# Performance work log

Measured on AMD Instinct MI355X. Metric: run time of the kernel, lower is better.

Reference implementation:

```python
import jax, jax.numpy as jnp
import numpy as np

FEAT_STRIDE = 16
NEG_OV, POS_OV = 0.3, 0.7
RPN_BATCH = 256
NUM_FG = int(0.5 * RPN_BATCH)  # RPN_FG_FRACTION * RPN_BATCHSIZE


def _gen_anchors(base=16, ratios=(0.5, 1.0, 2.0), scales=(4, 8, 16)):
    # 3D extension of the classic generate_anchors: ratio warps w/h, scale multiplies all dims
    ctr = (base - 1) / 2.0
    rows = []
    for r in ratios:
        for s in scales:
            w = base * s * np.sqrt(1.0 / r)
            h = base * s * np.sqrt(r)
            d = float(base * s)
            rows.append([ctr - 0.5 * (w - 1), ctr - 0.5 * (h - 1),
                         ctr + 0.5 * (w - 1), ctr + 0.5 * (h - 1),
                         ctr - 0.5 * (d - 1), ctr + 0.5 * (d - 1)])
    return np.asarray(rows, np.float32)


def setup_inputs() -> dict:
    key = jax.random.key(0)
    ks = jax.random.split(key, 8)
    B, H, W, D, K, A = 2, 48, 48, 24, 20, 9
    cls = jax.random.normal(ks[0], (B, 2 * A, H, W, D), jnp.float32)
    x1 = jax.random.uniform(ks[1], (B, K)) * 600.0
    y1 = jax.random.uniform(ks[2], (B, K)) * 600.0
    z1 = jax.random.uniform(ks[3], (B, K)) * 300.0
    whd = 16.0 + jax.random.uniform(ks[4], (B, K, 3)) * jnp.array([104.0, 104.0, 48.0])
    x2 = jnp.minimum(x1 + whd[..., 0], 767.0)
    y2 = jnp.minimum(y1 + whd[..., 1], 767.0)
    z2 = jnp.minimum(z1 + whd[..., 2], 383.0)
    cid = jax.random.randint(ks[5], (B, K), 1, 4).astype(jnp.float32)
    gt_boxes = jnp.stack([x1, y1, x2, y2, z1, z2, cid], axis=2)
    im_info = jnp.tile(jnp.array([[768.0, 768.0, 384.0]], jnp.float32), (B, 1))
    total = H * W * D * A
    return {
        'rpn_cls_score': cls,
        'gt_boxes': gt_boxes,
        'im_info': im_info,
        'num_boxes': jnp.full((B,), K, jnp.int32),
        'anchors': jnp.asarray(_gen_anchors()),
        'rand_fg': jax.random.uniform(ks[6], (B, total)),
        'rand_bg': jax.random.uniform(ks[7], (B, total)),
    }


def _overlaps(anc, gt):
    # anc: (N,6) [x1,y1,x2,y2,z1,z2]; gt: (B,K,7) -> IoU (B,N,K)
    aw = anc[:, 2] - anc[:, 0] + 1.0
    ah = anc[:, 3] - anc[:, 1] + 1.0
    ad = anc[:, 5] - anc[:, 4] + 1.0
    a_area = aw * ah * ad  # (N,)
    gw = gt[:, :, 2] - gt[:, :, 0] + 1.0
    gh = gt[:, :, 3] - gt[:, :, 1] + 1.0
    gd = gt[:, :, 5] - gt[:, :, 4] + 1.0
    g_area = gw * gh * gd  # (B,K)
    iw = jnp.clip(jnp.minimum(anc[None, :, None, 2], gt[:, None, :, 2]) -
                  jnp.maximum(anc[None, :, None, 0], gt[:, None, :, 0]) + 1.0, 0.0)
    ih = jnp.clip(jnp.minimum(anc[None, :, None, 3], gt[:, None, :, 3]) -
                  jnp.maximum(anc[None, :, None, 1], gt[:, None, :, 1]) + 1.0, 0.0)
    idp = jnp.clip(jnp.minimum(anc[None, :, None, 5], gt[:, None, :, 5]) -
                   jnp.maximum(anc[None, :, None, 4], gt[:, None, :, 4]) + 1.0, 0.0)
    inter = iw * ih * idp
    ov = inter / (a_area[None, :, None] + g_area[:, None, :] - inter)
    gt_zero = (gw == 1.0) & (gh == 1.0) & (gd == 1.0)
    a_zero = (aw == 1.0) & (ah == 1.0) & (ad == 1.0)
    ov = jnp.where(gt_zero[:, None, :], 0.0, ov)
    ov = jnp.where(a_zero[None, :, None], -1.0, ov)
    return ov


def _transform(ex, gt):
    # ex: (N,6); gt: (B,N,6) -> (B,N,6) targets (dx,dy,dz,dw,dh,dd)
    ew = ex[:, 2] - ex[:, 0] + 1.0
    eh = ex[:, 3] - ex[:, 1] + 1.0
    ed = ex[:, 5] - ex[:, 4] + 1.0
    ecx = ex[:, 0] + 0.5 * (ew - 1.0)
    ecy = ex[:, 1] + 0.5 * (eh - 1.0)
    ecz = ex[:, 4] + 0.5 * (ed - 1.0)
    gw = gt[:, :, 2] - gt[:, :, 0] + 1.0
    gh = gt[:, :, 3] - gt[:, :, 1] + 1.0
    gd = gt[:, :, 5] - gt[:, :, 4] + 1.0
    gcx = gt[:, :, 0] + 0.5 * (gw - 1.0)
    gcy = gt[:, :, 1] + 0.5 * (gh - 1.0)
    gcz = gt[:, :, 4] + 0.5 * (gd - 1.0)
    return jnp.stack([(gcx - ecx[None]) / ew[None],
                      (gcy - ecy[None]) / eh[None],
                      (gcz - ecz[None]) / ed[None],
                      jnp.log(gw / ew[None]),
                      jnp.log(gh / eh[None]),
                      jnp.log(gd / ed[None])], axis=2)


def _rank(p):
    # rank of each element when sorted by descending priority, per row
    return jnp.argsort(jnp.argsort(-p, axis=1), axis=1)


def reference(rpn_cls_score, gt_boxes, im_info, num_boxes, anchors, rand_fg, rand_bg):
    B = gt_boxes.shape[0]
    H, W, D = rpn_cls_score.shape[2], rpn_cls_score.shape[3], rpn_cls_score.shape[4]
    A = anchors.shape[0]
    sx = jnp.arange(W, dtype=jnp.float32) * FEAT_STRIDE
    sy = jnp.arange(H, dtype=jnp.float32) * FEAT_STRIDE
    sz = jnp.arange(D, dtype=jnp.float32) * FEAT_STRIDE
    mx, my, mz = jnp.meshgrid(sx, sy, sz, indexing='xy')  # (H,W,D) each
    shifts = jnp.stack([mx.ravel(), my.ravel(), mx.ravel(), my.ravel(), mz.ravel(), mz.ravel()], axis=1)
    all_anchors = (anchors[None, :, :] + shifts[:, None, :]).reshape(-1, 6)  # (total,6)
    total = all_anchors.shape[0]
    inside = ((all_anchors[:, 0] >= 0) & (all_anchors[:, 1] >= 0) & (all_anchors[:, 4] >= 0) &
              (all_anchors[:, 2] < im_info[0, 1]) & (all_anchors[:, 3] < im_info[0, 0]) &
              (all_anchors[:, 5] < im_info[0, 2]))  # (total,)

    ov = _overlaps(all_anchors, gt_boxes)                       # (B,total,K)
    ov_m = jnp.where(inside[None, :, None], ov, -1.0)           # mask outside anchors
    max_ov = ov_m.max(axis=2)
    argmax_ov = jnp.argmax(ov_m, axis=2)                        # (B,total)

    labels = jnp.full((B, total), -1.0, jnp.float32)
    ins = inside[None, :]
    labels = jnp.where(ins & (max_ov < NEG_OV), 0.0, labels)
    gt_max = ov_m.max(axis=1)                                   # (B,K)
    gt_max = jnp.where(gt_max == 0.0, 1e-5, gt_max)
    tie = jnp.sum(ov_m == gt_max[:, None, :], axis=2) > 0
    labels = jnp.where(ins & tie, 1.0, labels)
    labels = jnp.where(ins & (max_ov >= POS_OV), 1.0, labels)

    # fg subsampling: randomly keep at most NUM_FG positives per image
    fg = labels == 1.0
    rk = _rank(jnp.where(fg, rand_fg, -1.0))
    labels = jnp.where(fg & (rk >= NUM_FG), -1.0, labels)
    # bg subsampling: keep RPN_BATCH - num_fg negatives per image
    num_bg = RPN_BATCH - jnp.sum(labels == 1.0, axis=1)         # (B,)
    bg = labels == 0.0
    rkb = _rank(jnp.where(bg, rand_bg, -1.0))
    labels = jnp.where(bg & (rkb >= num_bg[:, None]), -1.0, labels)

    assigned = jnp.take_along_axis(gt_boxes, argmax_ov[:, :, None], axis=1)  # (B,total,7)
    bbox_targets = _transform(all_anchors, assigned[:, :, :6])
    bbox_targets = jnp.where(inside[None, :, None], bbox_targets, 0.0)

    in_w = jnp.where(labels == 1.0, 1.0, 0.0)                   # RPN_BBOX_INSIDE_WEIGHTS[0]=1
    # replicate original bug: weights from the LAST image's example count
    num_examples = jnp.sum(labels[-1] >= 0.0).astype(jnp.float32)
    w = 1.0 / num_examples
    out_w = jnp.where(labels == 1.0, w, jnp.where(labels == 0.0, w, 0.0))

    labels_o = labels.reshape(B, H, W, D, A).transpose(0, 4, 1, 2, 3).reshape(B, 1, A * H * D, W)
    bt_o = bbox_targets.reshape(B, H, W, D, A * 6).transpose(0, 4, 1, 2, 3)
    iw_o = jnp.broadcast_to(in_w[:, :, None], (B, total, 6)).reshape(B, H, W, D, 6 * A).transpose(0, 4, 1, 2, 3)
    ow_o = jnp.broadcast_to(out_w[:, :, None], (B, total, 6)).reshape(B, H, W, D, 6 * A).transpose(0, 4, 1, 2, 3)
    return labels_o, bt_o, iw_o, ow_o
```

## Files before the change

### kernel.cpp

```cpp
#include <hip/hip_runtime.h>
#include <math.h>

#define BB 2
#define HH 48
#define WW 48
#define DD 24
#define KK 20
#define AA 9
#define TOTAL (HH*WW*DD*AA)
#define SPAT (HH*WW*DD)
#define OUT0N (BB*TOTAL)
#define CH 54
#define NB 4096
#define CAP 4096
#define FG_QUOTA 128
#define RPN_B 256
#define STRIDE_F 16.0f

#define O_ARGMAX 0
#define O_GTMAX  (OUT0N)
#define O_HIST   (O_GTMAX + BB*KK)
#define O_CUT    (O_HIST + 4*NB)
#define O_TIEN   (O_CUT + 12)
#define O_TIE    (O_TIEN + 4)
#define O_W      (O_TIE + 4*CAP)

__device__ __forceinline__ unsigned enc_f(float f){
  unsigned u = __float_as_uint(f);
  return (u & 0x80000000u) ? ~u : (u | 0x80000000u);
}
__device__ __forceinline__ float dec_f(unsigned u){
  return (u & 0x80000000u) ? __uint_as_float(u & 0x7FFFFFFFu) : __uint_as_float(~u);
}
#define ENC_NEG1 0x407FFFFFu

__device__ __forceinline__ float iou6(float ax1,float ay1,float ax2,float ay2,
                                      float az1,float az2, const float* g){
  #pragma clang fp contract(off)
  float aw = ax2-ax1+1.0f, ah = ay2-ay1+1.0f, ad = az2-az1+1.0f;
  float a_area = aw*ah*ad;
  float gw = g[2]-g[0]+1.0f, gh = g[3]-g[1]+1.0f, gd = g[5]-g[4]+1.0f;
  float g_area = gw*gh*gd;
  float iw = fminf(ax2,g[2]) - fmaxf(ax1,g[0]) + 1.0f; iw = fmaxf(iw,0.0f);
  float ih = fminf(ay2,g[3]) - fmaxf(ay1,g[1]) + 1.0f; ih = fmaxf(ih,0.0f);
  float id = fminf(az2,g[5]) - fmaxf(az1,g[4]) + 1.0f; id = fmaxf(id,0.0f);
  float inter = iw*ih*id;
  float ov = inter / (a_area + g_area - inter);
  if (gw==1.0f && gh==1.0f && gd==1.0f) ov = 0.0f;
  if (aw==1.0f && ah==1.0f && ad==1.0f) ov = -1.0f;
  return ov;
}

__global__ void k_init(unsigned* __restrict__ ws){
  int t = blockIdx.x*256 + threadIdx.x;
  if (t < 4*NB) ws[O_HIST + t] = 0u;
  if (t < 4)    ws[O_TIEN + t] = 0u;
  if (t < BB*KK) ws[O_GTMAX + t] = ENC_NEG1;
}

#define GM_G 8
#define GM_BLK 243
__global__ void __launch_bounds__(256) k_gtmax(const float* __restrict__ gt,
    const float* __restrict__ anc, const float* __restrict__ imi,
    unsigned* __restrict__ ws){
  __shared__ float s_gt[KK*7];
  __shared__ float s_anc[AA*6];
  __shared__ float s_im[3];
  __shared__ unsigned s_max[KK];
  int tid = threadIdx.x;
  int b = blockIdx.y;
  for (int j=tid; j<KK*7; j+=256) s_gt[j] = gt[b*KK*7 + j];
  for (int j=tid; j<AA*6; j+=256) s_anc[j] = anc[j];
  if (tid<3) s_im[tid] = imi[tid];
  if (tid<KK) s_max[tid] = ENC_NEG1;
  __syncthreads();
  float rmax[KK];
  #pragma unroll
  for (int k=0;k<KK;k++) rmax[k] = -1.0f;
  int i0 = blockIdx.x*256 + tid;
  for (int g=0; g<GM_G; g++){
    int i = i0 + g*(GM_BLK*256);
    if (i >= TOTAL) break;
    int a = i % AA; int s = i / AA;
    int d = s % DD; int s2 = s / DD;
    int w = s2 % WW; int h = s2 / WW;
    float fx = w*STRIDE_F, fy = h*STRIDE_F, fz = d*STRIDE_F;
    float ax1=s_anc[a*6+0]+fx, ay1=s_anc[a*6+1]+fy, ax2=s_anc[a*6+2]+fx;
    float ay2=s_anc[a*6+3]+fy, az1=s_anc[a*6+4]+fz, az2=s_anc[a*6+5]+fz;
    bool inside = (ax1>=0.f)&&(ay1>=0.f)&&(az1>=0.f)&&
                  (ax2<s_im[1])&&(ay2<s_im[0])&&(az2<s_im[2]);
    if (!inside) continue;
    #pragma unroll
    for (int k=0;k<KK;k++)
      rmax[k] = fmaxf(rmax[k], iou6(ax1,ay1,ax2,ay2,az1,az2, &s_gt[k*7]));
  }
  #pragma unroll
  for (int k=0;k<KK;k++){
    float v = rmax[k];
    for (int off=32; off>0; off>>=1) v = fmaxf(v, __shfl_down(v, off, 64));
    if ((tid & 63) == 0) atomicMax(&s_max[k], enc_f(v));
  }
  __syncthreads();
  if (tid < KK) atomicMax(&ws[O_GTMAX + b*KK + tid], s_max[tid]);
}

__global__ void __launch_bounds__(256) k_label(const float* __restrict__ gt,
    const float* __restrict__ anc, const float* __restrict__ imi,
    const float* __restrict__ rfg, const float* __restrict__ rbg,
    float* __restrict__ out0, unsigned* __restrict__ ws){
  __shared__ float s_gt[BB*KK*7];
  __shared__ float s_anc[AA*6];
  __shared__ float s_im[3];
  __shared__ float s_gm[BB*KK];
  int tid = threadIdx.x;
  for (int j=tid; j<BB*KK*7; j+=256) s_gt[j] = gt[j];
  for (int j=tid; j<AA*6; j+=256) s_anc[j] = anc[j];
  if (tid<3) s_im[tid] = imi[tid];
  if (tid<BB*KK){ float g = dec_f(ws[O_GTMAX+tid]); if (g==0.0f) g = 1e-5f; s_gm[tid]=g; }
  __syncthreads();
  int t = blockIdx.x*256 + tid;
  if (t >= OUT0N) return;
  int d = t % DD; int r1 = t/DD;
  int w = r1 % WW; int r2 = r1/WW;
  int h = r2 % HH; int r3 = r2/HH;
  int a = r3 % AA; int b = r3/AA;
  int i = ((h*WW+w)*DD + d)*AA + a;
  float fx=w*STRIDE_F, fy=h*STRIDE_F, fz=d*STRIDE_F;
  float ax1=s_anc[a*6+0]+fx, ay1=s_anc[a*6+1]+fy, ax2=s_anc[a*6+2]+fx;
  float ay2=s_anc[a*6+3]+fy, az1=s_anc[a*6+4]+fz, az2=s_anc[a*6+5]+fz;
  bool inside = (ax1>=0.f)&&(ay1>=0.f)&&(az1>=0.f)&&
                (ax2<s_im[1])&&(ay2<s_im[0])&&(az2<s_im[2]);
  float L = -1.0f;
  int am = 0;
  if (inside){
    float mv = -2.0f; bool tie = false;
    #pragma unroll
    for (int k=0;k<KK;k++){
      float ov = iou6(ax1,ay1,ax2,ay2,az1,az2, &s_gt[(b*KK+k)*7]);
      if (ov > mv){ mv = ov; am = k; }
      tie = tie || (ov == s_gm[b*KK+k]);
    }
    if (mv < 0.3f) L = 0.0f;
    if (tie)       L = 1.0f;
    if (mv >= 0.7f) L = 1.0f;
  }
  out0[t] = L;
  ((int*)ws)[O_ARGMAX + t] = am;
  if (L == 1.0f){
    float r = rfg[b*TOTAL + i];
    int bk = min(NB-1, (int)(r*(float)NB));
    atomicAdd(&ws[O_HIST + b*NB + bk], 1u);
  } else if (L == 0.0f){
    float r = rbg[b*TOTAL + i];
    int bk = min(NB-1, (int)(r*(float)NB));
    atomicAdd(&ws[O_HIST + (2+b)*NB + bk], 1u);
  }
}

__global__ void __launch_bounds__(256) k_cuts(unsigned* __restrict__ ws){
  int fl = blockIdx.x; int tid = threadIdx.x;
  int b = fl & 1; int isbg = fl >> 1;
  const int CHK = NB/256;
  __shared__ unsigned ps[256];
  __shared__ unsigned s_fg;
  if (tid == 0) s_fg = 0u;
  __syncthreads();
  unsigned part = 0;
  int hi = NB - CHK*tid;
  for (int j = hi-CHK; j < hi; j++) part += ws[O_HIST + fl*NB + j];
  if (isbg){
    unsigned pf = 0;
    for (int j = tid*CHK; j < (tid+1)*CHK; j++) pf += ws[O_HIST + b*NB + j];
    atomicAdd(&s_fg, pf);
  }
  ps[tid] = part;
  __syncthreads();
  for (int off=1; off<256; off<<=1){
    unsigned v = (tid>=off) ? ps[tid-off] : 0u;
    __syncthreads();
    ps[tid] += v;
    __syncthreads();
  }
  unsigned N = ps[255];
  unsigned excl = ps[tid] - part;
  unsigned F = isbg ? s_fg : N;
  int quota = isbg ? (RPN_B - (int)min(F, (unsigned)FG_QUOTA)) : FG_QUOTA;
  if (fl == 3 && tid == 0){
    int fgk = min((int)F, FG_QUOTA);
    int bgk = min((int)N, RPN_B - fgk);
    ((float*)ws)[O_W] = 1.0f / (float)(fgk + bgk);
  }
  int* cut = (int*)&ws[O_CUT + fl*3];
  if ((int)N <= quota){
    if (tid==0){ cut[0] = -1; cut[1] = 0; cut[2] = quota; }
    return;
  }
  unsigned cum = excl;
  for (int bk = hi-1; bk >= hi-CHK; bk--){
    unsigned c = ws[O_HIST + fl*NB + bk];
    if (c > 0u && (unsigned)(quota-1) >= cum && (unsigned)(quota-1) < cum + c){
      cut[0] = bk; cut[1] = (int)cum; cut[2] = quota;
    }
    cum += c;
  }
}

__global__ void __launch_bounds__(256) k_apply(const float* __restrict__ rfg,
    const float* __restrict__ rbg, float* __restrict__ out0,
    unsigned* __restrict__ ws){
  int t = blockIdx.x*256 + threadIdx.x;
  if (t >= OUT0N) return;
  float L = out0[t];
  int isbg;
  if (L == 1.0f) isbg = 0; else if (L == 0.0f) isbg = 1; else return;
  int d = t % DD; int r1=t/DD; int w=r1%WW; int r2=r1/WW;
  int h = r2 % HH; int r3=r2/HH; int a=r3%AA; int b=r3/AA;
  int fl = isbg*2 + b;
  int cutb = ((int*)ws)[O_CUT + fl*3];
  if (cutb < 0) return;
  int i = ((h*WW+w)*DD + d)*AA + a;
  const float* ra = isbg ? rbg : rfg;
  float r = ra[b*TOTAL + i];
  int bk = min(NB-1, (int)(r*(float)NB));
  if (bk < cutb) out0[t] = -1.0f;
  else if (bk == cutb){
    unsigned pos = atomicAdd(&ws[O_TIEN + fl], 1u);
    if (pos < CAP) ((int*)ws)[O_TIE + fl*CAP + pos] = i;
  }
}

__global__ void __launch_bounds__(256) k_resolve(const float* __restrict__ rfg,
    const float* __restrict__ rbg, float* __restrict__ out0,
    unsigned* __restrict__ ws){
  int fl = blockIdx.x; int tid = threadIdx.x;
  int b = fl & 1; int isbg = fl >> 1;
  int cutb = ((int*)ws)[O_CUT + fl*3];
  if (cutb < 0) return;
  int rank_base = ((int*)ws)[O_CUT + fl*3 + 1];
  int quota     = ((int*)ws)[O_CUT + fl*3 + 2];
  int n = (int)min(ws[O_TIEN + fl], (unsigned)CAP);
  __shared__ float rv[CAP];
  __shared__ int   ri[CAP];
  const float* ra = isbg ? rbg : rfg;
  for (int e=tid; e<n; e+=256){
    int idx = ((int*)ws)[O_TIE + fl*CAP + e];
    ri[e] = idx; rv[e] = ra[b*TOTAL + idx];
  }
  __syncthreads();
  for (int e=tid; e<n; e+=256){
    float re = rv[e]; int ie = ri[e];
    int cnt = 0;
    for (int j=0; j<n; j++){
      float rj = rv[j];
      cnt += (rj > re) || (rj == re && ri[j] < ie);
    }
    if (rank_base + cnt >= quota){
      int a = ie % AA; int s = ie/AA; int d = s%DD; int s2 = s/DD;
      int w = s2 % WW; int h = s2 / WW;
      int o = (((b*AA+a)*HH + h)*WW + w)*DD + d;
      out0[o] = -1.0f;
    }
  }
}

__global__ void __launch_bounds__(256) k_out(const float* __restrict__ gt,
    const float* __restrict__ anc, const float* __restrict__ imi,
    const float* __restrict__ out0c, float* __restrict__ out,
    const unsigned* __restrict__ ws){
  __shared__ float s_gt[BB*KK*7];
  __shared__ float s_anc[AA*6];
  __shared__ float s_im[3];
  __shared__ float s_w;
  int tid = threadIdx.x;
  for (int j=tid; j<BB*KK*7; j+=256) s_gt[j] = gt[j];
  for (int j=tid; j<AA*6; j+=256) s_anc[j] = anc[j];
  if (tid<3) s_im[tid] = imi[tid];
  if (tid==0) s_w = ((const float*)ws)[O_W];
  __syncthreads();
  int t = blockIdx.x*256 + tid;
  if (t >= OUT0N) return;
  int d = t % DD; int r1=t/DD; int w=r1%WW; int r2=r1/WW;
  int h = r2 % HH; int r3=r2/HH; int a=r3%AA; int b=r3/AA;
  float L = out0c[t];
  int am = ((const int*)ws)[O_ARGMAX + t];
  float fx=w*STRIDE_F, fy=h*STRIDE_F, fz=d*STRIDE_F;
  float ax1=s_anc[a*6+0]+fx, ay1=s_anc[a*6+1]+fy, ax2=s_anc[a*6+2]+fx;
  float ay2=s_anc[a*6+3]+fy, az1=s_anc[a*6+4]+fz, az2=s_anc[a*6+5]+fz;
  bool inside = (ax1>=0.f)&&(ay1>=0.f)&&(az1>=0.f)&&
                (ax2<s_im[1])&&(ay2<s_im[0])&&(az2<s_im[2]);
  float bt[6] = {0.f,0.f,0.f,0.f,0.f,0.f};
  if (inside){
    const float* g = &s_gt[(b*KK + am)*7];
    float ew=ax2-ax1+1.f, eh=ay2-ay1+1.f, ed=az2-az1+1.f;
    float ecx=ax1+0.5f*(ew-1.f), ecy=ay1+0.5f*(eh-1.f), ecz=az1+0.5f*(ed-1.f);
    float gw=g[2]-g[0]+1.f, gh=g[3]-g[1]+1.f, gd=g[5]-g[4]+1.f;
    float gcx=g[0]+0.5f*(gw-1.f), gcy=g[1]+0.5f*(gh-1.f), gcz=g[4]+0.5f*(gd-1.f);
    bt[0]=(gcx-ecx)/ew; bt[1]=(gcy-ecy)/eh; bt[2]=(gcz-ecz)/ed;
    bt[3]=logf(gw/ew);  bt[4]=logf(gh/eh);  bt[5]=logf(gd/ed);
  }
  float iwv = (L==1.0f) ? 1.0f : 0.0f;
  float owv = (L==1.0f || L==0.0f) ? s_w : 0.0f;
  int sp = (h*WW + w)*DD + d;
  float* out1 = out + OUT0N;
  float* out2 = out1 + BB*CH*SPAT;
  float* out3 = out2 + BB*CH*SPAT;
  int basech = (b*CH + a*6)*SPAT + sp;
  #pragma unroll
  for (int c=0; c<6; c++){
    int off = basech + c*SPAT;
    out1[off] = bt[c];
    out2[off] = iwv;
    out3[off] = owv;
  }
}

extern "C" void kernel_launch(void* const* d_in, const int* in_sizes, int n_in,
                              void* d_out, int out_size, void* d_ws, size_t ws_size,
                              hipStream_t stream) {
  (void)in_sizes; (void)n_in; (void)out_size; (void)ws_size;
  const float* gt  = (const float*)d_in[1];
  const float* imi = (const float*)d_in[2];
  const float* anc = (const float*)d_in[4];
  const float* rfg = (const float*)d_in[5];
  const float* rbg = (const float*)d_in[6];
  float* out = (float*)d_out;
  unsigned* ws = (unsigned*)d_ws;
  int nb = (OUT0N + 255)/256;
  k_init   <<<dim3((4*NB+255)/256), dim3(256), 0, stream>>>(ws);
  k_gtmax  <<<dim3(GM_BLK, BB), dim3(256), 0, stream>>>(gt, anc, imi, ws);
  k_label  <<<dim3(nb), dim3(256), 0, stream>>>(gt, anc, imi, rfg, rbg, out, ws);
  k_cuts   <<<dim3(4), dim3(256), 0, stream>>>(ws);
  k_apply  <<<dim3(nb), dim3(256), 0, stream>>>(rfg, rbg, out, ws);
  k_resolve<<<dim3(4), dim3(256), 0, stream>>>(rfg, rbg, out, ws);
  k_out    <<<dim3(nb), dim3(256), 0, stream>>>(gt, anc, imi, out, out, ws);
}
```

Measured before the change: 189.3 us.

## Fuse subsampling into output kernel using per-bucket index lists and packed records

```diff
diff --git a/kernel.cpp b/kernel.cpp
--- a/kernel.cpp
+++ b/kernel.cpp
@@ -12,18 +12,17 @@
 #define OUT0N (BB*TOTAL)
 #define CH 54
 #define NB 4096
-#define CAP 4096
+#define CAPB 256
 #define FG_QUOTA 128
 #define RPN_B 256
 #define STRIDE_F 16.0f
 
-#define O_ARGMAX 0
+#define O_REC    0
 #define O_GTMAX  (OUT0N)
 #define O_HIST   (O_GTMAX + BB*KK)
 #define O_CUT    (O_HIST + 4*NB)
-#define O_TIEN   (O_CUT + 12)
-#define O_TIE    (O_TIEN + 4)
-#define O_W      (O_TIE + 4*CAP)
+#define O_W      (O_CUT + 16)
+#define O_LIST   (O_W + 1)
 
 __device__ __forceinline__ unsigned enc_f(float f){
   unsigned u = __float_as_uint(f);
@@ -51,13 +50,6 @@
   return ov;
 }
 
-__global__ void k_init(unsigned* __restrict__ ws){
-  int t = blockIdx.x*256 + threadIdx.x;
-  if (t < 4*NB) ws[O_HIST + t] = 0u;
-  if (t < 4)    ws[O_TIEN + t] = 0u;
-  if (t < BB*KK) ws[O_GTMAX + t] = ENC_NEG1;
-}
-
 #define GM_G 8
 #define GM_BLK 243
 __global__ void __launch_bounds__(256) k_gtmax(const float* __restrict__ gt,
@@ -69,6 +61,11 @@
   __shared__ unsigned s_max[KK];
   int tid = threadIdx.x;
   int b = blockIdx.y;
+  if (blockIdx.y == 0 && blockIdx.x < 16){
+    int base = blockIdx.x*256 + tid;
+    #pragma unroll
+    for (int j=0;j<4;j++) ws[O_HIST + j*NB + base] = 0u;
+  }
   for (int j=tid; j<KK*7; j+=256) s_gt[j] = gt[b*KK*7 + j];
   for (int j=tid; j<AA*6; j+=256) s_anc[j] = anc[j];
   if (tid<3) s_im[tid] = imi[tid];
@@ -80,7 +77,6 @@
   int i0 = blockIdx.x*256 + tid;
   for (int g=0; g<GM_G; g++){
     int i = i0 + g*(GM_BLK*256);
-    if (i >= TOTAL) break;
     int a = i % AA; int s = i / AA;
     int d = s % DD; int s2 = s / DD;
     int w = s2 % WW; int h = s2 / WW;
@@ -107,7 +103,7 @@
 __global__ void __launch_bounds__(256) k_label(const float* __restrict__ gt,
     const float* __restrict__ anc, const float* __restrict__ imi,
     const float* __restrict__ rfg, const float* __restrict__ rbg,
-    float* __restrict__ out0, unsigned* __restrict__ ws){
+    unsigned* __restrict__ ws){
   __shared__ float s_gt[BB*KK*7];
   __shared__ float s_anc[AA*6];
   __shared__ float s_im[3];
@@ -119,7 +115,6 @@
   if (tid<BB*KK){ float g = dec_f(ws[O_GTMAX+tid]); if (g==0.0f) g = 1e-5f; s_gm[tid]=g; }
   __syncthreads();
   int t = blockIdx.x*256 + tid;
-  if (t >= OUT0N) return;
   int d = t % DD; int r1 = t/DD;
   int w = r1 % WW; int r2 = r1/WW;
   int h = r2 % HH; int r3 = r2/HH;
@@ -144,17 +139,17 @@
     if (tie)       L = 1.0f;
     if (mv >= 0.7f) L = 1.0f;
   }
-  out0[t] = L;
-  ((int*)ws)[O_ARGMAX + t] = am;
-  if (L == 1.0f){
-    float r = rfg[b*TOTAL + i];
-    int bk = min(NB-1, (int)(r*(float)NB));
-    atomicAdd(&ws[O_HIST + b*NB + bk], 1u);
-  } else if (L == 0.0f){
-    float r = rbg[b*TOTAL + i];
-    int bk = min(NB-1, (int)(r*(float)NB));
-    atomicAdd(&ws[O_HIST + (2+b)*NB + bk], 1u);
-  }
+  unsigned code = (L==1.0f) ? 2u : ((L==0.0f) ? 1u : 0u);
+  unsigned bucket = 0;
+  if (code){
+    int fl = (code==1u ? 2 : 0) + b;
+    const float* ra = (code==1u) ? rbg : rfg;
+    float r = ra[b*TOTAL + i];
+    bucket = (unsigned)min(NB-1, (int)(r*(float)NB));
+    unsigned pos = atomicAdd(&ws[O_HIST + fl*NB + bucket], 1u);
+    if (pos < CAPB) ((int*)ws)[O_LIST + ((fl*NB + (int)bucket)<<8) + pos] = i;
+  }
+  ws[O_REC + t] = code | ((unsigned)am<<2) | (bucket<<7);
 }
 
 __global__ void __launch_bounds__(256) k_cuts(unsigned* __restrict__ ws){
@@ -190,83 +185,25 @@
     int bgk = min((int)N, RPN_B - fgk);
     ((float*)ws)[O_W] = 1.0f / (float)(fgk + bgk);
   }
-  int* cut = (int*)&ws[O_CUT + fl*3];
+  int* cut = (int*)&ws[O_CUT + fl*4];
   if ((int)N <= quota){
-    if (tid==0){ cut[0] = -1; cut[1] = 0; cut[2] = quota; }
+    if (tid==0){ cut[0] = -1; cut[1] = 0; cut[2] = quota; cut[3] = 0; }
     return;
   }
   unsigned cum = excl;
   for (int bk = hi-1; bk >= hi-CHK; bk--){
     unsigned c = ws[O_HIST + fl*NB + bk];
     if (c > 0u && (unsigned)(quota-1) >= cum && (unsigned)(quota-1) < cum + c){
-      cut[0] = bk; cut[1] = (int)cum; cut[2] = quota;
+      cut[0] = bk; cut[1] = (int)cum; cut[2] = quota; cut[3] = (int)c;
     }
     cum += c;
   }
 }
 
-__global__ void __launch_bounds__(256) k_apply(const float* __restrict__ rfg,
-    const float* __restrict__ rbg, float* __restrict__ out0,
-    unsigned* __restrict__ ws){
-  int t = blockIdx.x*256 + threadIdx.x;
-  if (t >= OUT0N) return;
-  float L = out0[t];
-  int isbg;
-  if (L == 1.0f) isbg = 0; else if (L == 0.0f) isbg = 1; else return;
-  int d = t % DD; int r1=t/DD; int w=r1%WW; int r2=r1/WW;
-  int h = r2 % HH; int r3=r2/HH; int a=r3%AA; int b=r3/AA;
-  int fl = isbg*2 + b;
-  int cutb = ((int*)ws)[O_CUT + fl*3];
-  if (cutb < 0) return;
-  int i = ((h*WW+w)*DD + d)*AA + a;
-  const float* ra = isbg ? rbg : rfg;
-  float r = ra[b*TOTAL + i];
-  int bk = min(NB-1, (int)(r*(float)NB));
-  if (bk < cutb) out0[t] = -1.0f;
-  else if (bk == cutb){
-    unsigned pos = atomicAdd(&ws[O_TIEN + fl], 1u);
-    if (pos < CAP) ((int*)ws)[O_TIE + fl*CAP + pos] = i;
-  }
-}
-
-__global__ void __launch_bounds__(256) k_resolve(const float* __restrict__ rfg,
-    const float* __restrict__ rbg, float* __restrict__ out0,
-    unsigned* __restrict__ ws){
-  int fl = blockIdx.x; int tid = threadIdx.x;
-  int b = fl & 1; int isbg = fl >> 1;
-  int cutb = ((int*)ws)[O_CUT + fl*3];
-  if (cutb < 0) return;
-  int rank_base = ((int*)ws)[O_CUT + fl*3 + 1];
-  int quota     = ((int*)ws)[O_CUT + fl*3 + 2];
-  int n = (int)min(ws[O_TIEN + fl], (unsigned)CAP);
-  __shared__ float rv[CAP];
-  __shared__ int   ri[CAP];
-  const float* ra = isbg ? rbg : rfg;
-  for (int e=tid; e<n; e+=256){
-    int idx = ((int*)ws)[O_TIE + fl*CAP + e];
-    ri[e] = idx; rv[e] = ra[b*TOTAL + idx];
-  }
-  __syncthreads();
-  for (int e=tid; e<n; e+=256){
-    float re = rv[e]; int ie = ri[e];
-    int cnt = 0;
-    for (int j=0; j<n; j++){
-      float rj = rv[j];
-      cnt += (rj > re) || (rj == re && ri[j] < ie);
-    }
-    if (rank_base + cnt >= quota){
-      int a = ie % AA; int s = ie/AA; int d = s%DD; int s2 = s/DD;
-      int w = s2 % WW; int h = s2 / WW;
-      int o = (((b*AA+a)*HH + h)*WW + w)*DD + d;
-      out0[o] = -1.0f;
-    }
-  }
-}
-
 __global__ void __launch_bounds__(256) k_out(const float* __restrict__ gt,
     const float* __restrict__ anc, const float* __restrict__ imi,
-    const float* __restrict__ out0c, float* __restrict__ out,
-    const unsigned* __restrict__ ws){
+    const float* __restrict__ rfg, const float* __restrict__ rbg,
+    float* __restrict__ out, const unsigned* __restrict__ ws){
   __shared__ float s_gt[BB*KK*7];
   __shared__ float s_anc[AA*6];
   __shared__ float s_im[3];
@@ -278,11 +215,37 @@
   if (tid==0) s_w = ((const float*)ws)[O_W];
   __syncthreads();
   int t = blockIdx.x*256 + tid;
-  if (t >= OUT0N) return;
   int d = t % DD; int r1=t/DD; int w=r1%WW; int r2=r1/WW;
   int h = r2 % HH; int r3=r2/HH; int a=r3%AA; int b=r3/AA;
-  float L = out0c[t];
-  int am = ((const int*)ws)[O_ARGMAX + t];
+  unsigned rec = ws[O_REC + t];
+  unsigned code = rec & 3u;
+  int am = (int)((rec>>2) & 31u);
+  int bucket = (int)((rec>>7) & 4095u);
+  float L = (code==2u) ? 1.0f : ((code==1u) ? 0.0f : -1.0f);
+  if (code){
+    int isbg = (code==1u);
+    int fl = isbg*2 + b;
+    const int* cut = (const int*)&ws[O_CUT + fl*4];
+    int cutb = cut[0];
+    if (cutb >= 0){
+      if (bucket < cutb) L = -1.0f;
+      else if (bucket == cutb){
+        int rank_base = cut[1], quota = cut[2];
+        int n = min(cut[3], CAPB);
+        int i = ((h*WW+w)*DD + d)*AA + a;
+        const float* ra = isbg ? rbg : rfg;
+        float ri = ra[b*TOTAL + i];
+        const int* lst = (const int*)ws + O_LIST + ((fl*NB + cutb)<<8);
+        int cnt = 0;
+        for (int e=0; e<n; e++){
+          int j = lst[e];
+          float rj = ra[b*TOTAL + j];
+          cnt += (rj > ri) || (rj == ri && j < i);
+        }
+        if (rank_base + cnt >= quota) L = -1.0f;
+      }
+    }
+  }
   float fx=w*STRIDE_F, fy=h*STRIDE_F, fz=d*STRIDE_F;
   float ax1=s_anc[a*6+0]+fx, ay1=s_anc[a*6+1]+fy, ax2=s_anc[a*6+2]+fx;
   float ay2=s_anc[a*6+3]+fy, az1=s_anc[a*6+4]+fz, az2=s_anc[a*6+5]+fz;
@@ -298,6 +261,7 @@
     bt[0]=(gcx-ecx)/ew; bt[1]=(gcy-ecy)/eh; bt[2]=(gcz-ecz)/ed;
     bt[3]=logf(gw/ew);  bt[4]=logf(gh/eh);  bt[5]=logf(gd/ed);
   }
+  out[t] = L;
   float iwv = (L==1.0f) ? 1.0f : 0.0f;
   float owv = (L==1.0f || L==0.0f) ? s_w : 0.0f;
   int sp = (h*WW + w)*DD + d;
@@ -326,11 +290,9 @@
   float* out = (float*)d_out;
   unsigned* ws = (unsigned*)d_ws;
   int nb = (OUT0N + 255)/256;
-  k_init   <<<dim3((4*NB+255)/256), dim3(256), 0, stream>>>(ws);
-  k_gtmax  <<<dim3(GM_BLK, BB), dim3(256), 0, stream>>>(gt, anc, imi, ws);
-  k_label  <<<dim3(nb), dim3(256), 0, stream>>>(gt, anc, imi, rfg, rbg, out, ws);
-  k_cuts   <<<dim3(4), dim3(256), 0, stream>>>(ws);
-  k_apply  <<<dim3(nb), dim3(256), 0, stream>>>(rfg, rbg, out, ws);
-  k_resolve<<<dim3(4), dim3(256), 0, stream>>>(rfg, rbg, out, ws);
-  k_out    <<<dim3(nb), dim3(256), 0, stream>>>(gt, anc, imi, out, out, ws);
-}
+  hipMemsetAsync((char*)d_ws + (size_t)O_GTMAX*4, 0, BB*KK*4, stream);
+  k_gtmax <<<dim3(GM_BLK, BB), dim3(256), 0, stream>>>(gt, anc, imi, ws);
+  k_label <<<dim3(nb), dim3(256), 0, stream>>>(gt, anc, imi, rfg, rbg, ws);
+  k_cuts  <<<dim3(4), dim3(256), 0, stream>>>(ws);
+  k_out   <<<dim3(nb), dim3(256), 0, stream>>>(gt, anc, imi, rfg, rbg, out, ws);
+}
```

Result: faster. 184.4 us (-2.5%).
